# Optimization experiments

Hardware: AMD Instinct MI355X
Metric: run time of the kernel (lower is better)

## Reference

```python
import jax, jax.numpy as jnp
import numpy as np

B, F_, J, D = 64, 256, 25, 3
FILT = 64
N = B * F_ * J
EPS = 1e-5


def setup_inputs() -> dict:
    key = jax.random.key(0)
    ks = jax.random.split(key, 20)
    x = jax.random.normal(ks[0], (B, F_, J, D), jnp.float32)
    # block-diagonal skeleton: chain bones, bidirectional, tiled over B*F graphs
    bones = np.stack([np.arange(J - 1), np.arange(1, J)], axis=1)  # (24,2)
    e = np.concatenate([bones, bones[:, ::-1]], axis=0)            # (48,2)
    G = B * F_
    off = (np.arange(G, dtype=np.int64) * J)[:, None, None]
    edge_index = jnp.asarray((e[None].astype(np.int64) + off).reshape(-1, 2).T)  # (2, G*48)
    s = 0.1
    W1 = jax.random.normal(ks[1], (D, FILT), jnp.float32) * s
    b1 = jnp.zeros((FILT,), jnp.float32)
    g1 = jnp.ones((FILT,), jnp.float32)
    be1 = jnp.zeros((FILT,), jnp.float32)
    W2 = jax.random.normal(ks[2], (FILT, FILT), jnp.float32) * s
    b2 = jnp.zeros((FILT,), jnp.float32)
    g2 = jnp.ones((FILT,), jnp.float32)
    be2 = jnp.zeros((FILT,), jnp.float32)
    cw1 = jax.random.normal(ks[3], (2 * FILT, J * FILT, 3), jnp.float32) * 0.02  # OIH
    cb1 = jnp.zeros((2 * FILT,), jnp.float32)
    cg1 = jnp.ones((2 * FILT,), jnp.float32)
    cbe1 = jnp.zeros((2 * FILT,), jnp.float32)
    cw2 = jax.random.normal(ks[4], (FILT, 2 * FILT, 1), jnp.float32) * 0.05
    cb2 = jnp.zeros((FILT,), jnp.float32)
    cg2 = jnp.ones((FILT,), jnp.float32)
    cbe2 = jnp.zeros((FILT,), jnp.float32)
    return dict(x=x, edge_index=edge_index, batch_size=B, frame_l=F_,
                W1=W1, b1=b1, g1=g1, be1=be1, W2=W2, b2=b2, g2=g2, be2=be2,
                cw1=cw1, cb1=cb1, cg1=cg1, cbe1=cbe1,
                cw2=cw2, cb2=cb2, cg2=cg2, cbe2=cbe2)


def _lrelu(v):
    return jnp.where(v >= 0, v, 0.2 * v)


def _bn_nodes(v, g, b):  # BatchNorm1d on (N, C), batch stats
    m = v.mean(0)
    var = v.var(0)
    return g * (v - m) * jax.lax.rsqrt(var + EPS) + b


def _bn_ncl(v, g, b):  # BatchNorm1d on (B, C, L), batch stats
    m = v.mean((0, 2), keepdims=True)
    var = v.var((0, 2), keepdims=True)
    return g[None, :, None] * (v - m) * jax.lax.rsqrt(var + EPS) + b[None, :, None]


def _gcn(h_in, W, b, src, dst, n):
    # PyG GCNConv: h' = D^{-1/2} (A+I) D^{-1/2} h W + b
    h = h_in @ W
    loop = jnp.arange(n, dtype=src.dtype)
    sa = jnp.concatenate([src, loop])
    da = jnp.concatenate([dst, loop])
    deg = jax.ops.segment_sum(jnp.ones(sa.shape[0], h.dtype), da, num_segments=n)
    dinv = jnp.where(deg > 0, jax.lax.rsqrt(deg), 0.0)
    norm = dinv[sa] * dinv[da]
    return jax.ops.segment_sum(h[sa] * norm[:, None], da, num_segments=n) + b


def _conv1d(v, w, pad):  # v:(B,C,L), w:(O,I,K)
    return jax.lax.conv_general_dilated(v, w, window_strides=(1,), padding=((pad, pad),),
                                         dimension_numbers=("NCH", "OIH", "NCH"))


def reference(x, edge_index, batch_size, frame_l, W1, b1, g1, be1, W2, b2, g2, be2,
              cw1, cb1, cg1, cbe1, cw2, cb2, cg2, cbe2):
    src, dst = edge_index[0], edge_index[1]
    n = x.shape[0] * x.shape[1] * x.shape[2]
    h = x.reshape(-1, x.shape[-1])                               # (N, D)
    h = _lrelu(_bn_nodes(_gcn(h, W1, b1, src, dst, n), g1, be1))  # (N, FILT)
    h = _lrelu(_bn_nodes(_gcn(h, W2, b2, src, dst, n), g2, be2))  # (N, FILT)
    t = h.reshape(batch_size, frame_l, -1).transpose(0, 2, 1)     # (B, J*FILT, L)
    t = _lrelu(_bn_ncl(_conv1d(t, cw1, 1) + cb1[None, :, None], cg1, cbe1))  # dropout: eval = identity
    t = _lrelu(_bn_ncl(_conv1d(t, cw2, 0) + cb2[None, :, None], cg2, cbe2))
    return t.transpose(0, 2, 1)                                   # (B, L, FILT)
```

## Files before the change

kernel.cpp:

```cpp
#include <hip/hip_runtime.h>
#include <stdint.h>

#define B_ 64
#define F2_ 256
#define J_ 25
#define FILT_ 64
#define C1_ 1600
#define O1_ 128
#define NN_ 409600
#define MM_ 16384
#define EPSV 1e-5f

typedef short short8 __attribute__((ext_vector_type(8)));
typedef float f32x4 __attribute__((ext_vector_type(4)));

static const size_t WS_Y2T  = 0;
static const size_t WS_XA   = 52838400;
static const size_t WS_WT1  = 57753600;
static const size_t WS_WT2  = 58982400;
static const size_t WS_WT2G = 58998784;
static const size_t WS_Y3   = 59006976;
static const size_t WS_H3   = 67395584;
static const size_t WS_Y4   = 71589888;
static const size_t WS_ST   = 75784192;
#define ST_S9    0
#define ST_SUM2  16
#define ST_SQ2   80
#define ST_SUM3  144
#define ST_SQ3   272
#define ST_SUM4  400
#define ST_SQ4   464
#define ST_S1    528
#define ST_T1    592
#define ST_SC2   656
#define ST_SH2   720
#define ST_SC3   784
#define ST_SH3   912
#define ST_SC4   1040
#define ST_SH4   1104
#define ST_COUNT 1168

__device__ __forceinline__ float bf2f(unsigned int u){
  return __uint_as_float(u << 16);
}
__device__ __forceinline__ unsigned short f2bf(float f){
  unsigned int u = __float_as_uint(f);
  u += 0x7fffu + ((u >> 16) & 1u);
  return (unsigned short)(u >> 16);
}
__device__ __forceinline__ float lrelu(float x){ return fmaxf(x, 0.2f * x); }
__device__ __forceinline__ float wsum(float v){
  #pragma unroll
  for (int off = 32; off > 0; off >>= 1) v += __shfl_down(v, off, 64);
  return v;
}

typedef __attribute__((address_space(3))) unsigned int lds_uint_t;
typedef __attribute__((address_space(1))) const unsigned int glob_uint_t;
__device__ __forceinline__ void gl16(const void* g, void* l){
  __builtin_amdgcn_global_load_lds((glob_uint_t*)g, (lds_uint_t*)l, 16, 0, 0);
}

__global__ __launch_bounds__(256) void k_zpad(unsigned short* __restrict__ y2t){
  int b = blockIdx.x, tid = threadIdx.x;
  if (tid < 200){
    uint4 z = make_uint4(0,0,0,0);
    ((uint4*)(y2t + (size_t)b * 412800))[tid] = z;
    ((uint4*)(y2t + (size_t)b * 412800 + 257 * 1600))[tid] = z;
  }
}

__global__ __launch_bounds__(256) void k_wt(const float* __restrict__ cw1,
                                            const float* __restrict__ W2,
                                            const float* __restrict__ cw2,
                                            unsigned short* __restrict__ wt1,
                                            unsigned short* __restrict__ wt2,
                                            unsigned short* __restrict__ wt2g){
  int blk = blockIdx.x;
  if (blk < 384){
    int k = blk >> 7, o = blk & 127;
    for (int c = threadIdx.x; c < 1600; c += 256)
      wt1[(size_t)(k * 128 + o) * 1600 + c] = f2bf(cw1[(size_t)(o * 1600 + c) * 3 + k]);
  } else if (blk < 416){
    int idx = ((blk - 384) << 8) + threadIdx.x;
    wt2[idx] = f2bf(cw2[idx]);
  } else {
    int idx = ((blk - 416) << 8) + threadIdx.x;
    int f = idx >> 6, cc = idx & 63;
    wt2g[idx] = f2bf(W2[cc * 64 + f]);
  }
}

__global__ __launch_bounds__(256) void k_gcn1(const float* __restrict__ x,
                                              float* __restrict__ xa,
                                              float* __restrict__ S9){
  int n = blockIdx.x * 256 + threadIdx.x;
  int j = n % J_;
  float dj  = (j == 0 || j == J_-1) ? 2.f : 3.f;
  float rdj = rsqrtf(dj);
  const float* xp = x + (size_t)n * 3;
  float wg = 1.f / dj;
  float a0 = xp[0]*wg, a1 = xp[1]*wg, a2 = xp[2]*wg;
  if (j > 0){
    float dm = (j == 1) ? 2.f : 3.f;  float w = rdj * rsqrtf(dm);
    a0 += xp[-3]*w; a1 += xp[-2]*w; a2 += xp[-1]*w;
  }
  if (j < J_-1){
    float dp = (j == J_-2) ? 2.f : 3.f;  float w = rdj * rsqrtf(dp);
    a0 += xp[3]*w; a1 += xp[4]*w; a2 += xp[5]*w;
  }
  float* xo = xa + (size_t)n * 3;
  xo[0] = a0; xo[1] = a1; xo[2] = a2;
  float p[9] = {a0, a1, a2, a0*a0, a0*a1, a0*a2, a1*a1, a1*a2, a2*a2};
  __shared__ float tmp[9][4];
  int wv = threadIdx.x >> 6, ln = threadIdx.x & 63;
  #pragma unroll
  for (int k = 0; k < 9; k++){ float s = wsum(p[k]); if (ln == 0) tmp[k][wv] = s; }
  __syncthreads();
  if (threadIdx.x < 9){
    int k = threadIdx.x;
    atomicAdd(S9 + k, tmp[k][0] + tmp[k][1] + tmp[k][2] + tmp[k][3]);
  }
}

__global__ void k_bn1(const float* __restrict__ S9, const float* __restrict__ W1,
                      const float* __restrict__ b1, const float* __restrict__ g1,
                      const float* __restrict__ be1,
                      float* __restrict__ s1, float* __restrict__ t1){
  int c = threadIdx.x;
  float inv = 1.f / (float)NN_;
  float m0 = S9[0]*inv, m1 = S9[1]*inv, m2 = S9[2]*inv;
  float C00 = S9[3]*inv - m0*m0, C01 = S9[4]*inv - m0*m1, C02 = S9[5]*inv - m0*m2;
  float C11 = S9[6]*inv - m1*m1, C12 = S9[7]*inv - m1*m2, C22 = S9[8]*inv - m2*m2;
  float w0 = W1[c], w1 = W1[64+c], w2 = W1[128+c];
  float mean = m0*w0 + m1*w1 + m2*w2 + b1[c];
  float var  = w0*w0*C00 + w1*w1*C11 + w2*w2*C22
             + 2.f*(w0*w1*C01 + w0*w2*C02 + w1*w2*C12);
  float s = g1[c] * rsqrtf(var + EPSV);
  s1[c] = s;
  t1[c] = be1[c] - s*mean + s*b1[c];
}

#define H1SLICE(ph, js) do { \
  int js_ = (js); \
  _Pragma("unroll") \
  for (int i_ = 0; i_ < 16; i_++){ \
    const float* xp_ = xas + ((size_t)(wl0 + i_) * 25 + js_) * 3; \
    h[ph][i_] = lrelu(fmaf(sS, fmaf(xp_[0], w0c, fmaf(xp_[1], w1c, xp_[2]*w2c)), tT)); \
  } } while(0)

#define AGGW(pm, pc, pp) do { \
  _Pragma("unroll") \
  for (int i_ = 0; i_ < 16; i_++){ \
    float a_ = wgm*h[pm][i_] + wgs*h[pc][i_] + wgp*h[pp][i_]; \
    int row_ = wl0 + i_; \
    *(unsigned short*)(As + row_*128 + ((((lane>>3)) ^ (row_&7))<<4) + ((lane&7)<<1)) = f2bf(a_); \
  } } while(0)

__global__ __launch_bounds__(256) void k_gcn2m(const float* __restrict__ xa,
                                               const float* __restrict__ W1,
                                               const float* __restrict__ s1,
                                               const float* __restrict__ t1,
                                               const float* __restrict__ b2,
                                               const unsigned short* __restrict__ wt2g,
                                               unsigned short* __restrict__ y2t,
                                               float* __restrict__ sum2,
                                               float* __restrict__ sq2){
  __shared__ float xas[4800];
  __shared__ float prm[384];
  __shared__ char As[8192];
  __shared__ char Bs[8192];
  int blk = blockIdx.x;
  int jh = blk & 1;
  int lq = (blk >> 1) & 3;
  int b  = blk >> 3;
  int l0 = lq << 6;
  int tid = threadIdx.x;
  int w = tid >> 6, lane = tid & 63;

  const float* xsrc = xa + (size_t)(b * 256 + l0) * 75;
  #pragma unroll
  for (int i = 0; i < 5; i++){
    int idx = tid + (i << 8);
    if (idx < 1200) ((float4*)xas)[idx] = ((const float4*)xsrc)[idx];
  }
  prm[tid] = (tid < 192) ? W1[tid] : s1[tid - 192];
  if (tid < 128) prm[256 + tid] = (tid < 64) ? t1[tid] : b2[tid - 64];
  #pragma unroll
  for (int i = 0; i < 2; i++){
    int r = (w << 4) + (i << 3) + (lane >> 3);
    int cblk = lane & 7;
    gl16(wt2g + (size_t)r * 64 + (((cblk ^ (r & 7))) << 3),
         Bs + (w << 11) + (i << 10));
  }
  __syncthreads();

  float w0c = prm[lane], w1c = prm[64 + lane], w2c = prm[128 + lane];
  float sS = prm[192 + lane], tT = prm[256 + lane];
  int wm = w >> 1, wn = w & 1;
  int m0 = (wm << 5) + (lane & 15);
  int n0 = (wn << 5) + (lane & 15);
  int kg = lane >> 4;
  float bias0 = prm[320 + n0], bias1 = prm[320 + n0 + 16];
  int wl0 = w << 4;

  float h[3][16];
  int J0 = jh ? 12 : 0;
  int NJ = jh ? 13 : 12;
  #pragma unroll
  for (int i = 0; i < 16; i++) h[2][i] = 0.f;
  H1SLICE(0, J0);
  if (J0 > 0) H1SLICE(2, J0 - 1);

  float ss0 = 0.f, ss1 = 0.f, qq0 = 0.f, qq1 = 0.f;

  #pragma unroll
  for (int jj = 0; jj < 13; jj++){
    if (jj >= NJ) break;
    int j = J0 + jj;
    if (j + 1 <= 24){
      switch ((jj + 1) % 3){
        case 0: H1SLICE(0, j + 1); break;
        case 1: H1SLICE(1, j + 1); break;
        case 2: H1SLICE(2, j + 1); break;
      }
    }
    float dj  = (j == 0 || j == 24) ? 2.f : 3.f;
    float rdj = rsqrtf(dj);
    float wgs = 1.f / dj;
    float wgm = (j > 0)  ? rdj * rsqrtf((j == 1)  ? 2.f : 3.f) : 0.f;
    float wgp = (j < 24) ? rdj * rsqrtf((j == 23) ? 2.f : 3.f) : 0.f;
    switch (jj % 3){
      case 0: AGGW(2, 0, 1); break;
      case 1: AGGW(0, 1, 2); break;
      case 2: AGGW(1, 2, 0); break;
    }
    __syncthreads();
    f32x4 acc[2][2] = {};
    #pragma unroll
    for (int ks = 0; ks < 2; ks++){
      int kb = kg + (ks << 2);
      short8 a0 = *(const short8*)(As + (m0 << 7)        + ((kb ^ (m0 & 7)) << 4));
      short8 a1 = *(const short8*)(As + ((m0 + 16) << 7) + ((kb ^ (m0 & 7)) << 4));
      short8 b0 = *(const short8*)(Bs + (n0 << 7)        + ((kb ^ (n0 & 7)) << 4));
      short8 b1 = *(const short8*)(Bs + ((n0 + 16) << 7) + ((kb ^ (n0 & 7)) << 4));
      acc[0][0] = __builtin_amdgcn_mfma_f32_16x16x32_bf16(a0, b0, acc[0][0], 0, 0, 0);
      acc[0][1] = __builtin_amdgcn_mfma_f32_16x16x32_bf16(a0, b1, acc[0][1], 0, 0, 0);
      acc[1][0] = __builtin_amdgcn_mfma_f32_16x16x32_bf16(a1, b0, acc[1][0], 0, 0, 0);
      acc[1][1] = __builtin_amdgcn_mfma_f32_16x16x32_bf16(a1, b1, acc[1][1], 0, 0, 0);
    }
    __syncthreads();
    int rowb = (wm << 5) + ((lane >> 4) << 2);
    #pragma unroll
    for (int mi = 0; mi < 2; mi++){
      #pragma unroll
      for (int ni = 0; ni < 2; ni++){
        float bias = ni ? bias1 : bias0;
        int f = n0 + (ni << 4);
        #pragma unroll
        for (int r = 0; r < 4; r++){
          float v = acc[mi][ni][r] + bias;
          if (ni){ ss1 += v; qq1 += v * v; } else { ss0 += v; qq0 += v * v; }
          int rl = rowb + (mi << 4) + r;
          y2t[(size_t)(b * 258 + l0 + rl + 1) * 1600 + j * 64 + f] = f2bf(v);
        }
      }
    }
  }
  ss0 += __shfl_xor(ss0, 16, 64); ss0 += __shfl_xor(ss0, 32, 64);
  ss1 += __shfl_xor(ss1, 16, 64); ss1 += __shfl_xor(ss1, 32, 64);
  qq0 += __shfl_xor(qq0, 16, 64); qq0 += __shfl_xor(qq0, 32, 64);
  qq1 += __shfl_xor(qq1, 16, 64); qq1 += __shfl_xor(qq1, 32, 64);
  if ((lane >> 4) == 0){
    atomicAdd(sum2 + n0, ss0);      atomicAdd(sq2 + n0, qq0);
    atomicAdd(sum2 + n0 + 16, ss1); atomicAdd(sq2 + n0 + 16, qq1);
  }
}

__global__ void k_bnp(const float* __restrict__ sum, const float* __restrict__ sq,
                      const float* __restrict__ g, const float* __restrict__ be,
                      float* __restrict__ sc, float* __restrict__ sh, float inv){
  int c = threadIdx.x;
  float mean = sum[c] * inv;
  float var  = sq[c] * inv - mean * mean;
  float s = g[c] * rsqrtf(var + EPSV);
  sc[c] = s; sh[c] = be[c] - s * mean;
}

__global__ __launch_bounds__(256) void k_bnapp2(unsigned short* __restrict__ y2t,
                                                const float* __restrict__ sc2,
                                                const float* __restrict__ sh2){
  for (unsigned idx = blockIdx.x * 256 + threadIdx.x; idx < 3276800u; idx += 524288u){
    unsigned b = idx / 51200u;
    unsigned rem = idx - b * 51200u;
    unsigned l = rem / 200u;
    unsigned cg = rem - l * 200u;
    uint4* p = (uint4*)y2t + ((size_t)b * 258 + l + 1) * 200 + cg;
    unsigned f0 = (cg << 3) & 63u;
    float4 sa = *(const float4*)(sc2 + f0);
    float4 sb = *(const float4*)(sc2 + f0 + 4);
    float4 ha = *(const float4*)(sh2 + f0);
    float4 hb = *(const float4*)(sh2 + f0 + 4);
    float scs[8] = {sa.x,sa.y,sa.z,sa.w,sb.x,sb.y,sb.z,sb.w};
    float shs[8] = {ha.x,ha.y,ha.z,ha.w,hb.x,hb.y,hb.z,hb.w};
    uint4 v = *p;
    unsigned vv[4] = {v.x,v.y,v.z,v.w};
    unsigned r[4];
    #pragma unroll
    for (int i = 0; i < 4; i++){
      float lo = bf2f(vv[i] & 0xffffu);
      float hi = bf2f(vv[i] >> 16);
      lo = lrelu(fmaf(scs[2*i],   lo, shs[2*i]));
      hi = lrelu(fmaf(scs[2*i+1], hi, shs[2*i+1]));
      r[i] = (unsigned)f2bf(lo) | (((unsigned)f2bf(hi)) << 16);
    }
    *p = make_uint4(r[0],r[1],r[2],r[3]);
  }
}

#define NT_ 75
__global__ __launch_bounds__(256) void k_conv1(const unsigned short* __restrict__ y2t,
                                               const unsigned short* __restrict__ wt1,
                                               const float* __restrict__ cb1,
                                               float* __restrict__ y3,
                                               float* __restrict__ sum3,
                                               float* __restrict__ sq3){
  __shared__ char smem[32768];
  int blk = blockIdx.x;
  int b  = blk >> 3;
  int lq = (blk >> 1) & 3;
  int og = blk & 1;
  int l0 = lq << 6;
  int tid = threadIdx.x;
  int w = tid >> 6, lane = tid & 63;
  int wm = w >> 1, wn = w & 1;
  const unsigned short* y2b = y2t + (size_t)b * 412800;
  const unsigned short* wtb = wt1 + (size_t)og * 64 * 1600;

  int rs = (w << 4) + (lane >> 3);
  int cblk = lane & 7;
  int m0 = (wm << 5) + (lane & 15);
  int n0 = (wn << 5) + (lane & 15);
  int kg = lane >> 4;

  f32x4 acc[2][2] = {};

  auto stage = [&](int t, int buf){
    int k = t / 25;
    int cc = (t - k * 25) << 6;
    const unsigned short* wk = wtb + (size_t)k * 204800;
    #pragma unroll
    for (int i = 0; i < 2; i++){
      int r = rs + (i << 3);
      int sw = (cblk ^ (r & 7)) << 3;
      gl16(y2b + (size_t)(l0 + r + k) * 1600 + cc + sw,
           smem + buf * 16384 + (w << 11) + (i << 10));
      gl16(wk + (size_t)r * 1600 + cc + sw,
           smem + buf * 16384 + 8192 + (w << 11) + (i << 10));
    }
  };

  stage(0, 0);
  __syncthreads();
  #pragma unroll 2
  for (int t = 0; t < NT_; ++t){
    int buf = t & 1;
    if (t + 1 < NT_) stage(t + 1, buf ^ 1);
    const char* Ab = smem + buf * 16384;
    const char* Bb = Ab + 8192;
    #pragma unroll
    for (int ks = 0; ks < 2; ks++){
      int kb = kg + (ks << 2);
      short8 a0 = *(const short8*)(Ab + (m0 << 7)        + ((kb ^ (m0 & 7)) << 4));
      short8 a1 = *(const short8*)(Ab + ((m0 + 16) << 7) + ((kb ^ (m0 & 7)) << 4));
      short8 b0 = *(const short8*)(Bb + (n0 << 7)        + ((kb ^ (n0 & 7)) << 4));
      short8 b1 = *(const short8*)(Bb + ((n0 + 16) << 7) + ((kb ^ (n0 & 7)) << 4));
      acc[0][0] = __builtin_amdgcn_mfma_f32_16x16x32_bf16(a0, b0, acc[0][0], 0, 0, 0);
      acc[0][1] = __builtin_amdgcn_mfma_f32_16x16x32_bf16(a0, b1, acc[0][1], 0, 0, 0);
      acc[1][0] = __builtin_amdgcn_mfma_f32_16x16x32_bf16(a1, b0, acc[1][0], 0, 0, 0);
      acc[1][1] = __builtin_amdgcn_mfma_f32_16x16x32_bf16(a1, b1, acc[1][1], 0, 0, 0);
    }
    __syncthreads();
  }

  int colb = (og << 6) + n0;
  int rowb = l0 + (wm << 5) + ((lane >> 4) << 2);
  float ss0 = 0.f, ss1 = 0.f, qq0 = 0.f, qq1 = 0.f;
  #pragma unroll
  for (int mi = 0; mi < 2; mi++){
    #pragma unroll
    for (int ni = 0; ni < 2; ni++){
      int col = colb + (ni << 4);
      float bias = cb1[col];
      #pragma unroll
      for (int r = 0; r < 4; r++){
        float v = acc[mi][ni][r] + bias;
        if (ni){ ss1 += v; qq1 += v * v; } else { ss0 += v; qq0 += v * v; }
        y3[(size_t)((b << 8) + rowb + (mi << 4) + r) * 128 + col] = v;
      }
    }
  }
  ss0 += __shfl_xor(ss0, 16, 64); ss0 += __shfl_xor(ss0, 32, 64);
  ss1 += __shfl_xor(ss1, 16, 64); ss1 += __shfl_xor(ss1, 32, 64);
  qq0 += __shfl_xor(qq0, 16, 64); qq0 += __shfl_xor(qq0, 32, 64);
  qq1 += __shfl_xor(qq1, 16, 64); qq1 += __shfl_xor(qq1, 32, 64);
  if ((lane >> 4) == 0){
    atomicAdd(sum3 + colb, ss0);      atomicAdd(sq3 + colb, qq0);
    atomicAdd(sum3 + colb + 16, ss1); atomicAdd(sq3 + colb + 16, qq1);
  }
}

__global__ __launch_bounds__(256) void k_h3(const float* __restrict__ y3,
                                            const float* __restrict__ sc3,
                                            const float* __restrict__ sh3,
                                            unsigned short* __restrict__ h3){
  unsigned q = blockIdx.x * 256 + threadIdx.x;
  unsigned o0 = (q & 31) << 2;
  float4 v = ((const float4*)y3)[q];
  float4 sc = *(const float4*)(sc3 + o0);
  float4 sh = *(const float4*)(sh3 + o0);
  float r0 = lrelu(fmaf(sc.x, v.x, sh.x));
  float r1 = lrelu(fmaf(sc.y, v.y, sh.y));
  float r2 = lrelu(fmaf(sc.z, v.z, sh.z));
  float r3 = lrelu(fmaf(sc.w, v.w, sh.w));
  uint2 u;
  u.x = (unsigned)f2bf(r0) | ((unsigned)f2bf(r1) << 16);
  u.y = (unsigned)f2bf(r2) | ((unsigned)f2bf(r3) << 16);
  ((uint2*)h3)[q] = u;
}

__global__ __launch_bounds__(256) void k_conv2(const unsigned short* __restrict__ h3,
                                               const unsigned short* __restrict__ wt2,
                                               const float* __restrict__ cb2,
                                               float* __restrict__ y4,
                                               float* __restrict__ sum4,
                                               float* __restrict__ sq4){
  __shared__ char smem[32768];
  int blk = blockIdx.x;
  int b = blk >> 2, lq = blk & 3;
  int l0 = lq << 6;
  int tid = threadIdx.x;
  int w = tid >> 6, lane = tid & 63;
  int wm = w >> 1, wn = w & 1;
  #pragma unroll
  for (int i = 0; i < 4; i++){
    int r = (w << 4) + (i << 2) + (lane >> 4);
    int sw = (((lane & 15) ^ (r & 7)) << 3);
    gl16(h3 + (size_t)((b << 8) + l0 + r) * 128 + sw, smem + (w << 12) + (i << 10));
    gl16(wt2 + (size_t)r * 128 + sw, smem + 16384 + (w << 12) + (i << 10));
  }
  __syncthreads();
  f32x4 acc[2][2] = {};
  int m0 = (wm << 5) + (lane & 15);
  int n0 = (wn << 5) + (lane & 15);
  int kg = lane >> 4;
  const char* Ab = smem;
  const char* Bb = smem + 16384;
  #pragma unroll
  for (int ks = 0; ks < 4; ks++){
    int kb = kg + (ks << 2);
    short8 a0 = *(const short8*)(Ab + (m0 << 8)        + ((kb ^ (m0 & 7)) << 4));
    short8 a1 = *(const short8*)(Ab + ((m0 + 16) << 8) + ((kb ^ (m0 & 7)) << 4));
    short8 b0 = *(const short8*)(Bb + (n0 << 8)        + ((kb ^ (n0 & 7)) << 4));
    short8 b1 = *(const short8*)(Bb + ((n0 + 16) << 8) + ((kb ^ (n0 & 7)) << 4));
    acc[0][0] = __builtin_amdgcn_mfma_f32_16x16x32_bf16(a0, b0, acc[0][0], 0, 0, 0);
    acc[0][1] = __builtin_amdgcn_mfma_f32_16x16x32_bf16(a0, b1, acc[0][1], 0, 0, 0);
    acc[1][0] = __builtin_amdgcn_mfma_f32_16x16x32_bf16(a1, b0, acc[1][0], 0, 0, 0);
    acc[1][1] = __builtin_amdgcn_mfma_f32_16x16x32_bf16(a1, b1, acc[1][1], 0, 0, 0);
  }
  int rowb = l0 + (wm << 5) + ((lane >> 4) << 2);
  float ss0 = 0.f, ss1 = 0.f, qq0 = 0.f, qq1 = 0.f;
  #pragma unroll
  for (int mi = 0; mi < 2; mi++){
    #pragma unroll
    for (int ni = 0; ni < 2; ni++){
      int f = n0 + (ni << 4);
      float bias = cb2[f];
      #pragma unroll
      for (int r = 0; r < 4; r++){
        float v = acc[mi][ni][r] + bias;
        if (ni){ ss1 += v; qq1 += v * v; } else { ss0 += v; qq0 += v * v; }
        y4[(size_t)((b << 8) + rowb + (mi << 4) + r) * 64 + f] = v;
      }
    }
  }
  ss0 += __shfl_xor(ss0, 16, 64); ss0 += __shfl_xor(ss0, 32, 64);
  ss1 += __shfl_xor(ss1, 16, 64); ss1 += __shfl_xor(ss1, 32, 64);
  qq0 += __shfl_xor(qq0, 16, 64); qq0 += __shfl_xor(qq0, 32, 64);
  qq1 += __shfl_xor(qq1, 16, 64); qq1 += __shfl_xor(qq1, 32, 64);
  if ((lane >> 4) == 0){
    atomicAdd(sum4 + n0, ss0);      atomicAdd(sq4 + n0, qq0);
    atomicAdd(sum4 + n0 + 16, ss1); atomicAdd(sq4 + n0 + 16, qq1);
  }
}

__global__ __launch_bounds__(256) void k_final(const float* __restrict__ y4,
                                               const float* __restrict__ sc4,
                                               const float* __restrict__ sh4,
                                               float* __restrict__ out){
  unsigned q = blockIdx.x * 256 + threadIdx.x;
  unsigned f0 = (q & 15) << 2;
  float4 v = ((const float4*)y4)[q];
  float4 sc = *(const float4*)(sc4 + f0);
  float4 sh = *(const float4*)(sh4 + f0);
  v.x = lrelu(fmaf(sc.x, v.x, sh.x));
  v.y = lrelu(fmaf(sc.y, v.y, sh.y));
  v.z = lrelu(fmaf(sc.z, v.z, sh.z));
  v.w = lrelu(fmaf(sc.w, v.w, sh.w));
  ((float4*)out)[q] = v;
}

extern "C" void kernel_launch(void* const* d_in, const int* in_sizes, int n_in,
                              void* d_out, int out_size, void* d_ws, size_t ws_size,
                              hipStream_t stream){
  const float* x    = (const float*)d_in[0];
  const float* W1   = (const float*)d_in[4];
  const float* b1   = (const float*)d_in[5];
  const float* g1   = (const float*)d_in[6];
  const float* be1  = (const float*)d_in[7];
  const float* W2   = (const float*)d_in[8];
  const float* b2   = (const float*)d_in[9];
  const float* g2   = (const float*)d_in[10];
  const float* be2  = (const float*)d_in[11];
  const float* cw1  = (const float*)d_in[12];
  const float* cb1  = (const float*)d_in[13];
  const float* cg1  = (const float*)d_in[14];
  const float* cbe1 = (const float*)d_in[15];
  const float* cw2  = (const float*)d_in[16];
  const float* cb2  = (const float*)d_in[17];
  const float* cg2  = (const float*)d_in[18];
  const float* cbe2 = (const float*)d_in[19];

  char* ws = (char*)d_ws;
  unsigned short* y2t  = (unsigned short*)(ws + WS_Y2T);
  float* xa            = (float*)(ws + WS_XA);
  unsigned short* wt1  = (unsigned short*)(ws + WS_WT1);
  unsigned short* wt2  = (unsigned short*)(ws + WS_WT2);
  unsigned short* wt2g = (unsigned short*)(ws + WS_WT2G);
  float* y3            = (float*)(ws + WS_Y3);
  unsigned short* h3   = (unsigned short*)(ws + WS_H3);
  float* y4            = (float*)(ws + WS_Y4);
  float* st            = (float*)(ws + WS_ST);

  if (ws_size < WS_ST + ST_COUNT * 4) return;

  hipMemsetAsync(st, 0, ST_COUNT * 4, stream);
  k_zpad  <<<64, 256, 0, stream>>>(y2t);
  k_wt    <<<432, 256, 0, stream>>>(cw1, W2, cw2, wt1, wt2, wt2g);
  k_gcn1  <<<1600, 256, 0, stream>>>(x, xa, st + ST_S9);
  k_bn1   <<<1, 64, 0, stream>>>(st + ST_S9, W1, b1, g1, be1, st + ST_S1, st + ST_T1);
  k_gcn2m <<<512, 256, 0, stream>>>(xa, W1, st + ST_S1, st + ST_T1, b2, wt2g,
                                    y2t, st + ST_SUM2, st + ST_SQ2);
  k_bnp   <<<1, 64, 0, stream>>>(st + ST_SUM2, st + ST_SQ2, g2, be2,
                                 st + ST_SC2, st + ST_SH2, 1.f / (float)NN_);
  k_bnapp2<<<2048, 256, 0, stream>>>(y2t, st + ST_SC2, st + ST_SH2);
  k_conv1 <<<512, 256, 0, stream>>>(y2t, wt1, cb1, y3, st + ST_SUM3, st + ST_SQ3);
  k_bnp   <<<1, 128, 0, stream>>>(st + ST_SUM3, st + ST_SQ3, cg1, cbe1,
                                  st + ST_SC3, st + ST_SH3, 1.f / (float)MM_);
  k_h3    <<<2048, 256, 0, stream>>>(y3, st + ST_SC3, st + ST_SH3, h3);
  k_conv2 <<<256, 256, 0, stream>>>(h3, wt2, cb2, y4, st + ST_SUM4, st + ST_SQ4);
  k_bnp   <<<1, 64, 0, stream>>>(st + ST_SUM4, st + ST_SQ4, cg2, cbe2,
                                 st + ST_SC4, st + ST_SH4, 1.f / (float)MM_);
  k_final <<<1024, 256, 0, stream>>>(y4, st + ST_SC4, st + ST_SH4, (float*)d_out);
}
```

Before: 192.9 us.

## Fuse BN3 apply into conv2 load and reorder conv1 block/K iteration

Removes the separate k_h3 kernel: conv2 now reads fp32 conv1 outputs, applies the BN scale/shift and leaky ReLU, converts to bf16 and writes directly into shared memory, eliminating the h3 intermediate buffer and one launch. conv1 blocks are remapped so that adjacent block IDs spread across batches and output groups, likely to improve cache/XCD locality. The conv1 K loop now iterates taps innermost within each channel chunk, so the same input rows are reused across consecutive stages. The fused load uses synchronous global loads instead of async LDS loads for the activation tile.

```diff
diff --git a/kernel.cpp b/kernel.cpp
--- a/kernel.cpp
+++ b/kernel.cpp
@@ -20,9 +20,8 @@
 static const size_t WS_WT2  = 58982400;
 static const size_t WS_WT2G = 58998784;
 static const size_t WS_Y3   = 59006976;
-static const size_t WS_H3   = 67395584;
-static const size_t WS_Y4   = 71589888;
-static const size_t WS_ST   = 75784192;
+static const size_t WS_Y4   = 67395584;
+static const size_t WS_ST   = 71589888;
 #define ST_S9    0
 #define ST_SUM2  16
 #define ST_SQ2   80
@@ -326,7 +325,8 @@
                                                float* __restrict__ sum3,
                                                float* __restrict__ sq3){
   __shared__ char smem[32768];
-  int blk = blockIdx.x;
+  int bid = blockIdx.x;
+  int blk = ((bid & 7) << 6) | (bid >> 3);
   int b  = blk >> 3;
   int lq = (blk >> 1) & 3;
   int og = blk & 1;
@@ -346,8 +346,9 @@
   f32x4 acc[2][2] = {};
 
   auto stage = [&](int t, int buf){
-    int k = t / 25;
-    int cc = (t - k * 25) << 6;
+    int cc6 = (t * 0x5556) >> 16;
+    int k   = t - cc6 * 3;
+    int cc  = cc6 << 6;
     const unsigned short* wk = wtb + (size_t)k * 204800;
     #pragma unroll
     for (int i = 0; i < 2; i++){
@@ -410,26 +411,9 @@
   }
 }
 
-__global__ __launch_bounds__(256) void k_h3(const float* __restrict__ y3,
-                                            const float* __restrict__ sc3,
-                                            const float* __restrict__ sh3,
-                                            unsigned short* __restrict__ h3){
-  unsigned q = blockIdx.x * 256 + threadIdx.x;
-  unsigned o0 = (q & 31) << 2;
-  float4 v = ((const float4*)y3)[q];
-  float4 sc = *(const float4*)(sc3 + o0);
-  float4 sh = *(const float4*)(sh3 + o0);
-  float r0 = lrelu(fmaf(sc.x, v.x, sh.x));
-  float r1 = lrelu(fmaf(sc.y, v.y, sh.y));
-  float r2 = lrelu(fmaf(sc.z, v.z, sh.z));
-  float r3 = lrelu(fmaf(sc.w, v.w, sh.w));
-  uint2 u;
-  u.x = (unsigned)f2bf(r0) | ((unsigned)f2bf(r1) << 16);
-  u.y = (unsigned)f2bf(r2) | ((unsigned)f2bf(r3) << 16);
-  ((uint2*)h3)[q] = u;
-}
-
-__global__ __launch_bounds__(256) void k_conv2(const unsigned short* __restrict__ h3,
+__global__ __launch_bounds__(256) void k_conv2(const float* __restrict__ y3,
+                                               const float* __restrict__ sc3,
+                                               const float* __restrict__ sh3,
                                                const unsigned short* __restrict__ wt2,
                                                const float* __restrict__ cb2,
                                                float* __restrict__ y4,
@@ -446,8 +430,29 @@
   for (int i = 0; i < 4; i++){
     int r = (w << 4) + (i << 2) + (lane >> 4);
     int sw = (((lane & 15) ^ (r & 7)) << 3);
-    gl16(h3 + (size_t)((b << 8) + l0 + r) * 128 + sw, smem + (w << 12) + (i << 10));
     gl16(wt2 + (size_t)r * 128 + sw, smem + 16384 + (w << 12) + (i << 10));
+  }
+  #pragma unroll
+  for (int i = 0; i < 4; i++){
+    int idx = tid + (i << 8);
+    int r = idx >> 4, s = idx & 15;
+    const float* src = y3 + (size_t)((b << 8) + l0 + r) * 128 + (s << 3);
+    float4 v0 = *(const float4*)(src);
+    float4 v1 = *(const float4*)(src + 4);
+    float4 c0 = *(const float4*)(sc3 + (s << 3));
+    float4 c1 = *(const float4*)(sc3 + (s << 3) + 4);
+    float4 h0 = *(const float4*)(sh3 + (s << 3));
+    float4 h1 = *(const float4*)(sh3 + (s << 3) + 4);
+    uint4 u;
+    u.x = (unsigned)f2bf(lrelu(fmaf(c0.x, v0.x, h0.x))) |
+          ((unsigned)f2bf(lrelu(fmaf(c0.y, v0.y, h0.y))) << 16);
+    u.y = (unsigned)f2bf(lrelu(fmaf(c0.z, v0.z, h0.z))) |
+          ((unsigned)f2bf(lrelu(fmaf(c0.w, v0.w, h0.w))) << 16);
+    u.z = (unsigned)f2bf(lrelu(fmaf(c1.x, v1.x, h1.x))) |
+          ((unsigned)f2bf(lrelu(fmaf(c1.y, v1.y, h1.y))) << 16);
+    u.w = (unsigned)f2bf(lrelu(fmaf(c1.z, v1.z, h1.z))) |
+          ((unsigned)f2bf(lrelu(fmaf(c1.w, v1.w, h1.w))) << 16);
+    *(uint4*)(smem + r * 256 + ((s ^ (r & 7)) << 4)) = u;
   }
   __syncthreads();
   f32x4 acc[2][2] = {};
@@ -538,7 +543,6 @@
   unsigned short* wt2  = (unsigned short*)(ws + WS_WT2);
   unsigned short* wt2g = (unsigned short*)(ws + WS_WT2G);
   float* y3            = (float*)(ws + WS_Y3);
-  unsigned short* h3   = (unsigned short*)(ws + WS_H3);
   float* y4            = (float*)(ws + WS_Y4);
   float* st            = (float*)(ws + WS_ST);
 
@@ -557,8 +561,8 @@
   k_conv1 <<<512, 256, 0, stream>>>(y2t, wt1, cb1, y3, st + ST_SUM3, st + ST_SQ3);
   k_bnp   <<<1, 128, 0, stream>>>(st + ST_SUM3, st + ST_SQ3, cg1, cbe1,
                                   st + ST_SC3, st + ST_SH3, 1.f / (float)MM_);
-  k_h3    <<<2048, 256, 0, stream>>>(y3, st + ST_SC3, st + ST_SH3, h3);
-  k_conv2 <<<256, 256, 0, stream>>>(h3, wt2, cb2, y4, st + ST_SUM4, st + ST_SQ4);
+  k_conv2 <<<256, 256, 0, stream>>>(y3, st + ST_SC3, st + ST_SH3, wt2, cb2,
+                                    y4, st + ST_SUM4, st + ST_SQ4);
   k_bnp   <<<1, 64, 0, stream>>>(st + ST_SUM4, st + ST_SQ4, cg2, cbe2,
                                  st + ST_SC4, st + ST_SH4, 1.f / (float)MM_);
   k_final <<<1024, 256, 0, stream>>>(y4, st + ST_SC4, st + ST_SH4, (float*)d_out);
```

Result: faster. 177.9 us (-7.8%).
